# Kernel tuning notes

Measured on AMD Instinct MI355X. Metric: run time of the kernel, lower is better.

## Reference

```python
import jax, jax.numpy as jnp
import numpy as np

MAX_SEQ = 768  # hardcoded in original compute_freqs_cis
THETA = 10000.0


def _freqs_cis(C, T):
    # freqs over FULL embed dim C (matches original, not per-head)
    freqs = 1.0 / THETA ** (jnp.arange(0, C, 2, dtype=jnp.float32)[: C // 2] / C)
    t = jnp.arange(MAX_SEQ, dtype=jnp.float32)
    ang = jnp.outer(t, freqs)  # [MAX_SEQ, C/2]
    return jnp.cos(ang)[:T], jnp.sin(ang)[:T]  # each [T, C/2]


def _apply_rope(u):
    # u: [B, T, C]; rotate adjacent channel pairs across full C
    B, T, C = u.shape
    fr, fi = _freqs_cis(C, T)           # [T, C/2]
    u2 = u.astype(jnp.float32).reshape(B, T, C // 2, 2)
    ur, ui = u2[..., 0], u2[..., 1]     # [B, T, C/2]
    out_r = ur * fr - ui * fi
    out_i = ur * fi + ui * fr
    return jnp.stack([out_r, out_i], axis=-1).reshape(B, T, C).astype(u.dtype)


def setup_inputs() -> dict:
    key = jax.random.key(0)
    k1, k2, k3 = jax.random.split(key, 3)
    B, T, C = 16, 768, 1024
    x = jax.random.normal(k1, (B, T, C), dtype=jnp.float32)
    Wqkv = jax.random.normal(k2, (3 * C, C), dtype=jnp.float32) * 0.02
    bqkv = jnp.zeros((3 * C,), dtype=jnp.float32)
    Wo = jax.random.normal(k3, (C, C), dtype=jnp.float32) * 0.02
    bo = jnp.zeros((C,), dtype=jnp.float32)
    return {"x": x, "Wqkv": Wqkv, "bqkv": bqkv, "Wo": Wo, "bo": bo}


def reference(x, Wqkv, bqkv, Wo, bo):
    B, T, C = x.shape
    H = 16
    D = C // H
    qkv = x @ Wqkv.T + bqkv                      # [B, T, 3C]
    q, k, v = jnp.split(qkv, 3, axis=-1)
    q = _apply_rope(q)
    k = _apply_rope(k)
    # [B, H, T, D]
    q = q.reshape(B, T, H, D).transpose(0, 2, 1, 3)
    k = k.reshape(B, T, H, D).transpose(0, 2, 1, 3)
    v = v.reshape(B, T, H, D).transpose(0, 2, 1, 3)
    scale = 1.0 / jnp.sqrt(jnp.asarray(D, dtype=q.dtype))
    scores = jnp.einsum("bhqd,bhkd->bhqk", q, k) * scale
    causal = jnp.tril(jnp.ones((T, T), dtype=bool))
    scores = jnp.where(causal, scores, jnp.finfo(scores.dtype).min)
    attn = jax.nn.softmax(scores, axis=-1)
    y = jnp.einsum("bhqk,bhkd->bhqd", attn, v)   # [B, H, T, D]
    y = y.transpose(0, 2, 1, 3).reshape(B, T, C)
    return y @ Wo.T + bo
```

## Files before the change

### kernel.cpp

```cpp
#include <hip/hip_runtime.h>
#include <hip/hip_bf16.h>

typedef __attribute__((ext_vector_type(8))) short bf16x8;
typedef __attribute__((ext_vector_type(4))) float f32x4;
typedef unsigned short u16;
typedef unsigned int u32;

#define DEV __device__ __forceinline__

DEV float bf2f(u16 v) { u32 u = ((u32)v) << 16; return __builtin_bit_cast(float, u); }
DEV u16 f2bf(float f) {
    u32 u = __builtin_bit_cast(u32, f);
    u32 r = (u + 0x7FFFu + ((u >> 16) & 1u)) >> 16;
    return (u16)r;
}

DEV void gll16(const u16* g, u16* l) {
    __builtin_amdgcn_global_load_lds((const __attribute__((address_space(1))) void*)g,
                                     (__attribute__((address_space(3))) void*)l, 16, 0, 0);
}

#define WAIT_VM0()   asm volatile("s_waitcnt vmcnt(0)" ::: "memory")
#define WAIT_LGKM0() asm volatile("s_waitcnt lgkmcnt(0)" ::: "memory")
#define BAR()        __builtin_amdgcn_s_barrier()
#define BARF()       asm volatile("s_barrier" ::: "memory")

__global__ void detect_kernel(const u32* __restrict__ x, int* __restrict__ flag) {
    __shared__ int cnt;
    if (threadIdx.x == 0) cnt = 0;
    __syncthreads();
    int c = 0;
    for (int i = threadIdx.x; i < 4096; i += 256) {
        u32 w = x[i];
        u32 e = (w >> 7) & 0xFF;
        c += (e >= 110 && e <= 132) ? 1 : 0;
    }
    atomicAdd(&cnt, c);
    __syncthreads();
    if (threadIdx.x == 0) *flag = (cnt * 2 > 4096) ? 1 : 0;
}

__global__ void cvt_bf16_kernel(const void* __restrict__ in, u16* __restrict__ out,
                                int n8, const int* __restrict__ flag) {
    const int fl = *flag;
    int i = blockIdx.x * 256 + threadIdx.x;
    const int stride = gridDim.x * 256;
    if (fl) {
        const bf16x8* ip = (const bf16x8*)in;
        bf16x8* op = (bf16x8*)out;
        for (; i < n8; i += stride) op[i] = ip[i];
    } else {
        const float4* ip = (const float4*)in;
        bf16x8* op = (bf16x8*)out;
        for (; i < n8; i += stride) {
            float4 a = ip[2 * i], b = ip[2 * i + 1];
            bf16x8 o;
            o[0] = (short)f2bf(a.x); o[1] = (short)f2bf(a.y);
            o[2] = (short)f2bf(a.z); o[3] = (short)f2bf(a.w);
            o[4] = (short)f2bf(b.x); o[5] = (short)f2bf(b.y);
            o[6] = (short)f2bf(b.z); o[7] = (short)f2bf(b.w);
            op[i] = o;
        }
    }
}

__global__ void cvt_f32_kernel(const void* __restrict__ in, float* __restrict__ out,
                               int n, const int* __restrict__ flag) {
    const int fl = *flag;
    int i = blockIdx.x * 256 + threadIdx.x;
    if (i < n) out[i] = fl ? bf2f(((const u16*)in)[i]) : ((const float*)in)[i];
}

__global__ void rope_table_kernel(float2* __restrict__ tab) {
    int idx = blockIdx.x * 256 + threadIdx.x;
    int t = idx >> 9, j = idx & 511;
    float freq = expf(-(float)(2 * j) * (9.210340371976184f / 1024.0f));
    float ang = (float)t * freq;
    tab[idx] = make_float2(cosf(ang), sinf(ang));
}

__global__ __launch_bounds__(256)
void gemm128_kernel(const u16* __restrict__ A, const u16* __restrict__ W,
                    const float* __restrict__ bias, void* __restrict__ C,
                    int N, const int* __restrict__ flag, int out_mode,
                    const float2* __restrict__ tab, int rope) {
    constexpr int K = 1024, NT = 16;
    __shared__ u16 lds[2][16384];
    const int tid = threadIdx.x;
    const int l = tid & 63, w = tid >> 6;
    const int wm = w >> 1, wn = w & 1;
    const int lo = l & 15, hi = l >> 4;

    const int M0 = blockIdx.x * 128, N0 = blockIdx.y * 128;

    const int rS = tid >> 3;
    const int qS = (tid & 7) ^ (rS & 7);
    const u16* Ag = A + (size_t)(M0 + rS) * K + qS * 8;
    const u16* Wg = W + (size_t)(N0 + rS) * K + qS * 8;
    const int lb = w * 512;

    f32x4 acc[4][4] = {};

#define STAGE(kt, slot)                                                        \
    {                                                                          \
        u16* sA = &lds[slot][0];                                               \
        u16* sB = &lds[slot][8192];                                            \
        const u16* ga = Ag + (kt) * 64;                                        \
        const u16* gb = Wg + (kt) * 64;                                        \
        gll16(ga,                   sA + lb);                                  \
        gll16(ga + (size_t)32 * K,  sA + 2048 + lb);                           \
        gll16(ga + (size_t)64 * K,  sA + 4096 + lb);                           \
        gll16(ga + (size_t)96 * K,  sA + 6144 + lb);                           \
        gll16(gb,                   sB + lb);                                  \
        gll16(gb + (size_t)32 * K,  sB + 2048 + lb);                           \
        gll16(gb + (size_t)64 * K,  sB + 4096 + lb);                           \
        gll16(gb + (size_t)96 * K,  sB + 6144 + lb);                           \
    }

    STAGE(0, 0);
    WAIT_VM0();
    BARF();

#pragma unroll 1
    for (int j = 0; j < NT; ++j) {
        const int cur = j & 1;
        if (j + 1 < NT) STAGE(j + 1, cur ^ 1);

        const u16* sA = &lds[cur][0];
        const u16* sB = &lds[cur][8192];
        bf16x8 a[4][2], b[4][2];
#pragma unroll
        for (int m = 0; m < 4; ++m)
#pragma unroll
            for (int ks = 0; ks < 2; ++ks)
                a[m][ks] = *(const bf16x8*)&sA[(wm * 64 + m * 16 + lo) * 64 +
                                               (((ks * 4 + hi) ^ (lo & 7)) * 8)];
#pragma unroll
        for (int n = 0; n < 4; ++n)
#pragma unroll
            for (int ks = 0; ks < 2; ++ks)
                b[n][ks] = *(const bf16x8*)&sB[(wn * 64 + n * 16 + lo) * 64 +
                                               (((ks * 4 + hi) ^ (lo & 7)) * 8)];
        __builtin_amdgcn_s_setprio(1);
#pragma unroll
        for (int m = 0; m < 4; ++m)
#pragma unroll
            for (int n = 0; n < 4; ++n)
#pragma unroll
                for (int ks = 0; ks < 2; ++ks)
                    acc[m][n] = __builtin_amdgcn_mfma_f32_16x16x32_bf16(a[m][ks], b[n][ks], acc[m][n], 0, 0, 0);
        __builtin_amdgcn_s_setprio(0);

        if (j + 1 < NT) WAIT_VM0();
        BARF();
    }
#undef STAGE

    const int f32out = out_mode ? (*flag == 0) : 0;
    const int do_rope = rope && (N0 < 2048);
    const int row0 = M0 + wm * 64 + hi * 4;
    const int col0 = N0 + wn * 64 + lo;
    const int t0 = (M0 % 768) + wm * 64 + hi * 4;
#pragma unroll
    for (int n = 0; n < 4; ++n) {
        const int col = col0 + n * 16;
        float bi = bias[col];
        const int jf = (col & 1023) >> 1;
        const int odd = col & 1;
#pragma unroll
        for (int m = 0; m < 4; ++m)
#pragma unroll
            for (int j = 0; j < 4; ++j) {
                float v = acc[m][n][j] + bi;
                if (do_rope) {
                    float partner = __shfl_xor(v, 1);
                    float2 cs = tab[(t0 + m * 16 + j) * 512 + jf];
                    v = odd ? (v * cs.x + partner * cs.y) : (v * cs.x - partner * cs.y);
                }
                size_t idx = (size_t)(row0 + m * 16 + j) * N + col;
                if (f32out) ((float*)C)[idx] = v;
                else        ((u16*)C)[idx] = f2bf(v);
            }
    }
}

__global__ __launch_bounds__(256)
void attn_kernel(const u16* __restrict__ qkv, u16* __restrict__ y) {
    constexpr int T = 768, CH = 1024, QKVC = 3072;
    constexpr float NEG = -30000.0f;
    __shared__ u16 Ks[2][64 * 64];
    __shared__ u16 Vt[64 * 72];
    __shared__ u16 Ps[64 * 72];

    const int tid = threadIdx.x, l = tid & 63, w = tid >> 6;
    const int qt = blockIdx.x, h = blockIdx.y, b = blockIdx.z;
    const int lo = l & 15, hi = l >> 4;
    const int kk = hi * 8;
    const int swzk = (lo & 7) * 8;

    const int qrow = qt * 64 + w * 16 + lo;
    const u16* qptr = qkv + (size_t)(b * T + qrow) * QKVC + h * 64 + kk;
    bf16x8 aq0r = *(const bf16x8*)qptr;
    bf16x8 aq1r = *(const bf16x8*)(qptr + 32);
    bf16x8 aq0, aq1;
#pragma unroll
    for (int e = 0; e < 8; ++e) {
        aq0[e] = (short)f2bf(bf2f((u16)aq0r[e]) * 0.125f);
        aq1[e] = (short)f2bf(bf2f((u16)aq1r[e]) * 0.125f);
    }

    f32x4 o[4] = {};
    float mrun[4] = {NEG, NEG, NEG, NEG};
    float lrun[4] = {0.f, 0.f, 0.f, 0.f};

    const int ksr = w * 16 + (l >> 3);
    const int ksc = ((l & 7) ^ ((l >> 3) & 7)) * 8;
    const u16* kbase = qkv + (size_t)(b * T + ksr) * QKVC + CH + h * 64 + ksc;

    const int vd0 = (tid & 7) * 8;
    const int vswz = (tid & 7) * 8;
    const int vr0 = tid >> 3, vr1 = 32 + (tid >> 3);
    const u16* vbase = qkv + (size_t)(b * T) * QKVC + 2 * CH + h * 64 + vd0;

    gll16(kbase, &Ks[0][w * 1024]);
    gll16(kbase + (size_t)8 * QKVC, &Ks[0][w * 1024 + 512]);
    bf16x8 cv0 = *(const bf16x8*)(vbase + (size_t)vr0 * QKVC);
    bf16x8 cv1 = *(const bf16x8*)(vbase + (size_t)vr1 * QKVC);
    WAIT_VM0();
#pragma unroll
    for (int e = 0; e < 8; ++e) {
        Vt[(vd0 + e) * 72 + (vr0 ^ vswz)] = (u16)cv0[e];
        Vt[(vd0 + e) * 72 + (vr1 ^ vswz)] = (u16)cv1[e];
    }

    for (int kt = 0; kt <= qt; ++kt) {
        const int cur = kt & 1, nxt = cur ^ 1;
        bf16x8 nv0, nv1;
        if (kt < qt) {
            const size_t koff = (size_t)((kt + 1) * 64) * QKVC;
            gll16(kbase + koff, &Ks[nxt][w * 1024]);
            gll16(kbase + koff + (size_t)8 * QKVC, &Ks[nxt][w * 1024 + 512]);
            const u16* vb2 = vbase + (size_t)((kt + 1) * 64) * QKVC;
            nv0 = *(const bf16x8*)(vb2 + (size_t)vr0 * QKVC);
            nv1 = *(const bf16x8*)(vb2 + (size_t)vr1 * QKVC);
        }
        WAIT_LGKM0();
        BAR();

        __builtin_amdgcn_s_setprio(1);
        f32x4 s[4];
#pragma unroll
        for (int n = 0; n < 4; ++n) {
            bf16x8 kb0 = *(const bf16x8*)&Ks[cur][(n * 16 + lo) * 64 + (kk ^ swzk)];
            bf16x8 kb1 = *(const bf16x8*)&Ks[cur][(n * 16 + lo) * 64 + ((32 + kk) ^ swzk)];
            f32x4 z = {0.f, 0.f, 0.f, 0.f};
            z = __builtin_amdgcn_mfma_f32_16x16x32_bf16(aq0, kb0, z, 0, 0, 0);
            z = __builtin_amdgcn_mfma_f32_16x16x32_bf16(aq1, kb1, z, 0, 0, 0);
            s[n] = z;
        }
        __builtin_amdgcn_s_setprio(0);

        if (kt == qt) {
#pragma unroll
            for (int n = 0; n < 4; ++n) {
                int kcol = n * 16 + lo;
#pragma unroll
                for (int j = 0; j < 4; ++j)
                    if (kcol > w * 16 + hi * 4 + j) s[n][j] = NEG;
            }
        }
        float mnew[4], corr[4];
#pragma unroll
        for (int j = 0; j < 4; ++j) {
            float mx = fmaxf(fmaxf(s[0][j], s[1][j]), fmaxf(s[2][j], s[3][j]));
            mx = fmaxf(mx, __shfl_xor(mx, 1));
            mx = fmaxf(mx, __shfl_xor(mx, 2));
            mx = fmaxf(mx, __shfl_xor(mx, 4));
            mx = fmaxf(mx, __shfl_xor(mx, 8));
            mnew[j] = fmaxf(mrun[j], mx);
            corr[j] = __expf(mrun[j] - mnew[j]);
            mrun[j] = mnew[j];
        }
        float p[4][4];
#pragma unroll
        for (int n = 0; n < 4; ++n)
#pragma unroll
            for (int j = 0; j < 4; ++j)
                p[n][j] = __expf(s[n][j] - mnew[j]);
#pragma unroll
        for (int j = 0; j < 4; ++j) {
            float r = p[0][j] + p[1][j] + p[2][j] + p[3][j];
            r += __shfl_xor(r, 1);
            r += __shfl_xor(r, 2);
            r += __shfl_xor(r, 4);
            r += __shfl_xor(r, 8);
            lrun[j] = lrun[j] * corr[j] + r;
        }
#pragma unroll
        for (int n = 0; n < 4; ++n)
#pragma unroll
            for (int j = 0; j < 4; ++j)
                o[n][j] *= corr[j];
#pragma unroll
        for (int n = 0; n < 4; ++n)
#pragma unroll
            for (int j = 0; j < 4; ++j)
                Ps[(w * 16 + hi * 4 + j) * 72 + n * 16 + lo] = f2bf(p[n][j]);

        __builtin_amdgcn_s_setprio(1);
#pragma unroll
        for (int c = 0; c < 2; ++c) {
            bf16x8 pa = *(const bf16x8*)&Ps[(w * 16 + lo) * 72 + c * 32 + kk];
#pragma unroll
            for (int n = 0; n < 4; ++n) {
                const int v = (n * 2 + (lo >> 3)) & 7;
                bf16x8 vb = *(const bf16x8*)&Vt[(n * 16 + lo) * 72 + ((c * 32 + kk) ^ (v * 8))];
                o[n] = __builtin_amdgcn_mfma_f32_16x16x32_bf16(pa, vb, o[n], 0, 0, 0);
            }
        }
        __builtin_amdgcn_s_setprio(0);

        if (kt < qt) {
            WAIT_VM0();
            BAR();
#pragma unroll
            for (int e = 0; e < 8; ++e) {
                Vt[(vd0 + e) * 72 + (vr0 ^ vswz)] = (u16)nv0[e];
                Vt[(vd0 + e) * 72 + (vr1 ^ vswz)] = (u16)nv1[e];
            }
        }
    }

    float inv[4];
#pragma unroll
    for (int j = 0; j < 4; ++j) inv[j] = (lrun[j] > 0.f) ? 1.0f / lrun[j] : 0.f;
#pragma unroll
    for (int n = 0; n < 4; ++n)
#pragma unroll
        for (int j = 0; j < 4; ++j) {
            int t = qt * 64 + w * 16 + hi * 4 + j;
            y[(size_t)(b * T + t) * CH + h * 64 + n * 16 + lo] = f2bf(o[n][j] * inv[j]);
        }
}

extern "C" void kernel_launch(void* const* d_in, const int* in_sizes, int n_in,
                              void* d_out, int out_size, void* d_ws, size_t ws_size,
                              hipStream_t stream) {
    char* ws = (char*)d_ws;
    int*   flag  = (int*)ws;
    u16*   xb    = (u16*)(ws + 256);
    u16*   Wqb   = (u16*)(ws + 256 + 25165824);
    u16*   Wob   = (u16*)(ws + 256 + 31457280);
    float* bqf   = (float*)(ws + 256 + 33554432);
    float* bof   = (float*)(ws + 256 + 33566720);
    u16*   qkv   = (u16*)(ws + 256 + 33570816);
    u16*   y     = (u16*)(ws + 256 + 109068288);
    float2* tab  = (float2*)(ws + 256 + 134234112);

    detect_kernel<<<1, 256, 0, stream>>>((const u32*)d_in[0], flag);
    cvt_bf16_kernel<<<2048, 256, 0, stream>>>(d_in[0], xb,  12582912 / 8, flag);
    cvt_bf16_kernel<<<1536, 256, 0, stream>>>(d_in[1], Wqb, 3145728 / 8, flag);
    cvt_bf16_kernel<<<512,  256, 0, stream>>>(d_in[3], Wob, 1048576 / 8, flag);
    cvt_f32_kernel<<<12, 256, 0, stream>>>(d_in[2], bqf, 3072, flag);
    cvt_f32_kernel<<<4,  256, 0, stream>>>(d_in[4], bof, 1024, flag);
    rope_table_kernel<<<768 * 512 / 256, 256, 0, stream>>>(tab);

    gemm128_kernel<<<dim3(96, 24), 256, 0, stream>>>(xb, Wqb, bqf, qkv, 3072, flag, 0, tab, 1);
    attn_kernel<<<dim3(12, 16, 16), 256, 0, stream>>>(qkv, y);
    gemm128_kernel<<<dim3(96, 8), 256, 0, stream>>>(y, Wob, bof, d_out, 1024, flag, 1, tab, 0);
}
```

Measured before the change: 316.3 us.

## Use 256x128 tile GEMM with triple-buffered LDS for QKV projection

Adds a 512-thread GEMM kernel with a 256x128 output tile and a three-slot LDS ring that prefetches two K-tiles ahead, using a partial vmcnt wait instead of a full drain. It replaces the 128x128 kernel for the QKV projection. The aim is more reuse of each W tile per block and better overlap of global loads with MFMA work. In exchange it uses about 144KB of LDS per block, which may cap occupancy at one block per CU, and launches half as many blocks.

```diff
diff --git a/kernel.cpp b/kernel.cpp
--- a/kernel.cpp
+++ b/kernel.cpp
@@ -21,6 +21,7 @@
 }
 
 #define WAIT_VM0()   asm volatile("s_waitcnt vmcnt(0)" ::: "memory")
+#define WAIT_VM6()   asm volatile("s_waitcnt vmcnt(6)" ::: "memory")
 #define WAIT_LGKM0() asm volatile("s_waitcnt lgkmcnt(0)" ::: "memory")
 #define BAR()        __builtin_amdgcn_s_barrier()
 #define BARF()       asm volatile("s_barrier" ::: "memory")
@@ -79,6 +80,110 @@
     tab[idx] = make_float2(cosf(ang), sinf(ang));
 }
 
+__global__ __launch_bounds__(512)
+void gemm256_kernel(const u16* __restrict__ A, const u16* __restrict__ W,
+                    const float* __restrict__ bias, void* __restrict__ C,
+                    int N, const int* __restrict__ flag, int out_mode,
+                    const float2* __restrict__ tab, int rope) {
+    constexpr int K = 1024, NT = 16;
+    __shared__ u16 lds[3][24576];
+    const int tid = threadIdx.x;
+    const int l = tid & 63, w = tid >> 6;
+    const int wm = w >> 1, wn = w & 1;
+    const int lo = l & 15, hi = l >> 4;
+
+    const int M0 = blockIdx.x * 256, N0 = blockIdx.y * 128;
+
+    const int rS = tid >> 3;
+    const int qS = (tid & 7) ^ (rS & 7);
+    const u16* Ag = A + (size_t)(M0 + rS) * K + qS * 8;
+    const u16* Wg = W + (size_t)(N0 + rS) * K + qS * 8;
+    const int lb = w * 512;
+
+    f32x4 acc[4][4] = {};
+
+#define STAGE(kt, slot)                                                        \
+    {                                                                          \
+        u16* sA = &lds[slot][0];                                               \
+        u16* sB = &lds[slot][16384];                                           \
+        const u16* ga = Ag + (kt) * 64;                                        \
+        const u16* gb = Wg + (kt) * 64;                                        \
+        gll16(ga,                       sA + lb);                              \
+        gll16(ga + (size_t)64 * K,      sA + 4096 + lb);                       \
+        gll16(ga + (size_t)128 * K,     sA + 8192 + lb);                       \
+        gll16(ga + (size_t)192 * K,     sA + 12288 + lb);                      \
+        gll16(gb,                       sB + lb);                              \
+        gll16(gb + (size_t)64 * K,      sB + 4096 + lb);                       \
+    }
+
+    STAGE(0, 0);
+    STAGE(1, 1);
+    WAIT_VM6();
+
+#pragma unroll 1
+    for (int j = 0; j < NT; ++j) {
+        BAR();
+        if (j + 2 < NT) {
+            STAGE(j + 2, (j + 2) % 3);
+            WAIT_VM6();
+        } else {
+            WAIT_VM0();
+        }
+        const u16* sA = &lds[j % 3][0];
+        const u16* sB = &lds[j % 3][16384];
+        bf16x8 a[4][2], b[4][2];
+#pragma unroll
+        for (int m = 0; m < 4; ++m)
+#pragma unroll
+            for (int ks = 0; ks < 2; ++ks)
+                a[m][ks] = *(const bf16x8*)&sA[(wm * 64 + m * 16 + lo) * 64 +
+                                               (((ks * 4 + hi) ^ (lo & 7)) * 8)];
+#pragma unroll
+        for (int n = 0; n < 4; ++n)
+#pragma unroll
+            for (int ks = 0; ks < 2; ++ks)
+                b[n][ks] = *(const bf16x8*)&sB[(wn * 64 + n * 16 + lo) * 64 +
+                                               (((ks * 4 + hi) ^ (lo & 7)) * 8)];
+        __builtin_amdgcn_s_setprio(1);
+#pragma unroll
+        for (int m = 0; m < 4; ++m)
+#pragma unroll
+            for (int n = 0; n < 4; ++n)
+#pragma unroll
+                for (int ks = 0; ks < 2; ++ks)
+                    acc[m][n] = __builtin_amdgcn_mfma_f32_16x16x32_bf16(a[m][ks], b[n][ks], acc[m][n], 0, 0, 0);
+        __builtin_amdgcn_s_setprio(0);
+    }
+#undef STAGE
+
+    const int f32out = out_mode ? (*flag == 0) : 0;
+    const int do_rope = rope && (N0 < 2048);
+    const int row0 = M0 + wm * 64 + hi * 4;
+    const int col0 = N0 + wn * 64 + lo;
+    const int t0 = (M0 % 768) + wm * 64 + hi * 4;
+#pragma unroll
+    for (int n = 0; n < 4; ++n) {
+        const int col = col0 + n * 16;
+        float bi = bias[col];
+        const int jf = (col & 1023) >> 1;
+        const int odd = col & 1;
+#pragma unroll
+        for (int m = 0; m < 4; ++m)
+#pragma unroll
+            for (int j = 0; j < 4; ++j) {
+                float v = acc[m][n][j] + bi;
+                if (do_rope) {
+                    float partner = __shfl_xor(v, 1);
+                    float2 cs = tab[(t0 + m * 16 + j) * 512 + jf];
+                    v = odd ? (v * cs.x + partner * cs.y) : (v * cs.x - partner * cs.y);
+                }
+                size_t idx = (size_t)(row0 + m * 16 + j) * N + col;
+                if (f32out) ((float*)C)[idx] = v;
+                else        ((u16*)C)[idx] = f2bf(v);
+            }
+    }
+}
+
 __global__ __launch_bounds__(256)
 void gemm128_kernel(const u16* __restrict__ A, const u16* __restrict__ W,
                     const float* __restrict__ bias, void* __restrict__ C,
@@ -365,7 +470,7 @@
     cvt_f32_kernel<<<4,  256, 0, stream>>>(d_in[4], bof, 1024, flag);
     rope_table_kernel<<<768 * 512 / 256, 256, 0, stream>>>(tab);
 
-    gemm128_kernel<<<dim3(96, 24), 256, 0, stream>>>(xb, Wqb, bqf, qkv, 3072, flag, 0, tab, 1);
+    gemm256_kernel<<<dim3(48, 24), 512, 0, stream>>>(xb, Wqb, bqf, qkv, 3072, flag, 0, tab, 1);
     attn_kernel<<<dim3(12, 16, 16), 256, 0, stream>>>(qkv, y);
     gemm128_kernel<<<dim3(96, 8), 256, 0, stream>>>(y, Wob, bof, d_out, 1024, flag, 1, tab, 0);
 }
```

New measurement: 325.2 us. 1.03x slower.

## Replace 128x128 GEMM with 256x256 tile, 8-wave ping-pong pipelined kernel

Applied to the files above, without the earlier changes.

The QKV and output projection GEMMs move from a 128x128 tile with 4 waves to a 256x256 tile with 8 waves, and each wave now computes 128x64. The K-loop is split into four MFMA phases separated by barriers, with the A and B loads for the next stage issued between phases so loads overlap compute. The aim is more operand reuse per LDS byte and better latency hiding. In exchange the kernel needs 128KB of LDS per block and more accumulator registers, and it launches fewer blocks (576 and 192), so wave quantization across CUs is a risk, especially for the output GEMM.

```diff
diff --git a/kernel.cpp b/kernel.cpp
--- a/kernel.cpp
+++ b/kernel.cpp
@@ -79,19 +79,19 @@
     tab[idx] = make_float2(cosf(ang), sinf(ang));
 }
 
-__global__ __launch_bounds__(256)
-void gemm128_kernel(const u16* __restrict__ A, const u16* __restrict__ W,
-                    const float* __restrict__ bias, void* __restrict__ C,
-                    int N, const int* __restrict__ flag, int out_mode,
-                    const float2* __restrict__ tab, int rope) {
+__global__ __launch_bounds__(512, 2)
+void gemm256p_kernel(const u16* __restrict__ A, const u16* __restrict__ W,
+                     const float* __restrict__ bias, void* __restrict__ C,
+                     int N, const int* __restrict__ flag, int out_mode,
+                     const float2* __restrict__ tab, int rope) {
     constexpr int K = 1024, NT = 16;
-    __shared__ u16 lds[2][16384];
+    __shared__ u16 lds[2][32768];
     const int tid = threadIdx.x;
     const int l = tid & 63, w = tid >> 6;
-    const int wm = w >> 1, wn = w & 1;
+    const int wm = w >> 2, wn = w & 3;
     const int lo = l & 15, hi = l >> 4;
 
-    const int M0 = blockIdx.x * 128, N0 = blockIdx.y * 128;
+    const int M0 = blockIdx.x * 256, N0 = blockIdx.y * 256;
 
     const int rS = tid >> 3;
     const int qS = (tid & 7) ^ (rS & 7);
@@ -99,88 +99,126 @@
     const u16* Wg = W + (size_t)(N0 + rS) * K + qS * 8;
     const int lb = w * 512;
 
-    f32x4 acc[4][4] = {};
-
-#define STAGE(kt, slot)                                                        \
+    f32x4 acc[8][4] = {};
+
+#define STG_A(kt, slot, half)                                                  \
     {                                                                          \
-        u16* sA = &lds[slot][0];                                               \
-        u16* sB = &lds[slot][8192];                                            \
-        const u16* ga = Ag + (kt) * 64;                                        \
-        const u16* gb = Wg + (kt) * 64;                                        \
-        gll16(ga,                   sA + lb);                                  \
-        gll16(ga + (size_t)32 * K,  sA + 2048 + lb);                           \
-        gll16(ga + (size_t)64 * K,  sA + 4096 + lb);                           \
-        gll16(ga + (size_t)96 * K,  sA + 6144 + lb);                           \
-        gll16(gb,                   sB + lb);                                  \
-        gll16(gb + (size_t)32 * K,  sB + 2048 + lb);                           \
-        gll16(gb + (size_t)64 * K,  sB + 4096 + lb);                           \
-        gll16(gb + (size_t)96 * K,  sB + 6144 + lb);                           \
-    }
-
-    STAGE(0, 0);
+        u16* sA_ = &lds[slot][(half) * 8192];                                  \
+        const u16* ga_ = Ag + (kt) * 64 + (size_t)(128 * (half)) * K;          \
+        gll16(ga_,                  sA_ + lb);                                 \
+        gll16(ga_ + (size_t)64 * K, sA_ + 4096 + lb);                          \
+    }
+#define STG_B(kt, slot, half)                                                  \
+    {                                                                          \
+        u16* sB_ = &lds[slot][16384 + (half) * 8192];                          \
+        const u16* gb_ = Wg + (kt) * 64 + (size_t)(128 * (half)) * K;          \
+        gll16(gb_,                  sB_ + lb);                                 \
+        gll16(gb_ + (size_t)64 * K, sB_ + 4096 + lb);                          \
+    }
+
+    STG_A(0, 0, 0); STG_A(0, 0, 1);
+    STG_B(0, 0, 0); STG_B(0, 0, 1);
     WAIT_VM0();
     BARF();
 
+    const int csw = lo & 7;
+
 #pragma unroll 1
-    for (int j = 0; j < NT; ++j) {
-        const int cur = j & 1;
-        if (j + 1 < NT) STAGE(j + 1, cur ^ 1);
-
+    for (int t = 0; t < NT; ++t) {
+        const int cur = t & 1, nxt = cur ^ 1;
         const u16* sA = &lds[cur][0];
-        const u16* sB = &lds[cur][8192];
-        bf16x8 a[4][2], b[4][2];
-#pragma unroll
-        for (int m = 0; m < 4; ++m)
-#pragma unroll
-            for (int ks = 0; ks < 2; ++ks)
-                a[m][ks] = *(const bf16x8*)&sA[(wm * 64 + m * 16 + lo) * 64 +
-                                               (((ks * 4 + hi) ^ (lo & 7)) * 8)];
+        const u16* sB = &lds[cur][16384];
+        bf16x8 afr[4], bfr[4];
+
 #pragma unroll
         for (int n = 0; n < 4; ++n)
-#pragma unroll
-            for (int ks = 0; ks < 2; ++ks)
-                b[n][ks] = *(const bf16x8*)&sB[(wn * 64 + n * 16 + lo) * 64 +
-                                               (((ks * 4 + hi) ^ (lo & 7)) * 8)];
+            bfr[n] = *(const bf16x8*)&sB[(wn * 64 + n * 16 + lo) * 64 + ((hi ^ csw) * 8)];
+#pragma unroll
+        for (int m = 0; m < 4; ++m)
+            afr[m] = *(const bf16x8*)&sA[(wm * 128 + m * 16 + lo) * 64 + ((hi ^ csw) * 8)];
+        if (t + 1 < NT) { STG_A(t + 1, nxt, 0); STG_A(t + 1, nxt, 1); }
+        BARF();
         __builtin_amdgcn_s_setprio(1);
 #pragma unroll
         for (int m = 0; m < 4; ++m)
 #pragma unroll
             for (int n = 0; n < 4; ++n)
-#pragma unroll
-                for (int ks = 0; ks < 2; ++ks)
-                    acc[m][n] = __builtin_amdgcn_mfma_f32_16x16x32_bf16(a[m][ks], b[n][ks], acc[m][n], 0, 0, 0);
-        __builtin_amdgcn_s_setprio(0);
-
-        if (j + 1 < NT) WAIT_VM0();
-        BARF();
-    }
-#undef STAGE
+                acc[m][n] = __builtin_amdgcn_mfma_f32_16x16x32_bf16(afr[m], bfr[n], acc[m][n], 0, 0, 0);
+        __builtin_amdgcn_s_setprio(0);
+        BARF();
+
+#pragma unroll
+        for (int m = 0; m < 4; ++m)
+            afr[m] = *(const bf16x8*)&sA[(wm * 128 + 64 + m * 16 + lo) * 64 + ((hi ^ csw) * 8)];
+        if (t + 1 < NT) { STG_B(t + 1, nxt, 0); STG_B(t + 1, nxt, 1); }
+        BARF();
+        __builtin_amdgcn_s_setprio(1);
+#pragma unroll
+        for (int m = 0; m < 4; ++m)
+#pragma unroll
+            for (int n = 0; n < 4; ++n)
+                acc[4 + m][n] = __builtin_amdgcn_mfma_f32_16x16x32_bf16(afr[m], bfr[n], acc[4 + m][n], 0, 0, 0);
+        __builtin_amdgcn_s_setprio(0);
+        BARF();
+
+#pragma unroll
+        for (int n = 0; n < 4; ++n)
+            bfr[n] = *(const bf16x8*)&sB[(wn * 64 + n * 16 + lo) * 64 + (((4 + hi) ^ csw) * 8)];
+#pragma unroll
+        for (int m = 0; m < 4; ++m)
+            afr[m] = *(const bf16x8*)&sA[(wm * 128 + m * 16 + lo) * 64 + (((4 + hi) ^ csw) * 8)];
+        BARF();
+        __builtin_amdgcn_s_setprio(1);
+#pragma unroll
+        for (int m = 0; m < 4; ++m)
+#pragma unroll
+            for (int n = 0; n < 4; ++n)
+                acc[m][n] = __builtin_amdgcn_mfma_f32_16x16x32_bf16(afr[m], bfr[n], acc[m][n], 0, 0, 0);
+        __builtin_amdgcn_s_setprio(0);
+        BARF();
+
+#pragma unroll
+        for (int m = 0; m < 4; ++m)
+            afr[m] = *(const bf16x8*)&sA[(wm * 128 + 64 + m * 16 + lo) * 64 + (((4 + hi) ^ csw) * 8)];
+        WAIT_VM0();
+        BARF();
+        __builtin_amdgcn_s_setprio(1);
+#pragma unroll
+        for (int m = 0; m < 4; ++m)
+#pragma unroll
+            for (int n = 0; n < 4; ++n)
+                acc[4 + m][n] = __builtin_amdgcn_mfma_f32_16x16x32_bf16(afr[m], bfr[n], acc[4 + m][n], 0, 0, 0);
+        __builtin_amdgcn_s_setprio(0);
+        BARF();
+    }
+#undef STG_A
+#undef STG_B
 
     const int f32out = out_mode ? (*flag == 0) : 0;
     const int do_rope = rope && (N0 < 2048);
-    const int row0 = M0 + wm * 64 + hi * 4;
-    const int col0 = N0 + wn * 64 + lo;
-    const int t0 = (M0 % 768) + wm * 64 + hi * 4;
-#pragma unroll
-    for (int n = 0; n < 4; ++n) {
-        const int col = col0 + n * 16;
-        float bi = bias[col];
-        const int jf = (col & 1023) >> 1;
-        const int odd = col & 1;
-#pragma unroll
-        for (int m = 0; m < 4; ++m)
+#pragma unroll
+    for (int mi = 0; mi < 8; ++mi) {
+        const int rbase = M0 + wm * 128 + (mi >> 2) * 64 + (mi & 3) * 16 + hi * 4;
+        const int tbase = (M0 % 768) + wm * 128 + (mi >> 2) * 64 + (mi & 3) * 16 + hi * 4;
+#pragma unroll
+        for (int n = 0; n < 4; ++n) {
+            const int col = N0 + wn * 64 + lo + n * 16;
+            float bi = bias[col];
+            const int jf = (col & 1023) >> 1;
+            const int odd = col & 1;
 #pragma unroll
             for (int j = 0; j < 4; ++j) {
-                float v = acc[m][n][j] + bi;
+                float v = acc[mi][n][j] + bi;
                 if (do_rope) {
                     float partner = __shfl_xor(v, 1);
-                    float2 cs = tab[(t0 + m * 16 + j) * 512 + jf];
+                    float2 cs = tab[(tbase + j) * 512 + jf];
                     v = odd ? (v * cs.x + partner * cs.y) : (v * cs.x - partner * cs.y);
                 }
-                size_t idx = (size_t)(row0 + m * 16 + j) * N + col;
+                size_t idx = (size_t)(rbase + j) * N + col;
                 if (f32out) ((float*)C)[idx] = v;
                 else        ((u16*)C)[idx] = f2bf(v);
             }
+        }
     }
 }
 
@@ -365,7 +403,7 @@
     cvt_f32_kernel<<<4,  256, 0, stream>>>(d_in[4], bof, 1024, flag);
     rope_table_kernel<<<768 * 512 / 256, 256, 0, stream>>>(tab);
 
-    gemm128_kernel<<<dim3(96, 24), 256, 0, stream>>>(xb, Wqb, bqf, qkv, 3072, flag, 0, tab, 1);
+    gemm256p_kernel<<<dim3(48, 12), 512, 0, stream>>>(xb, Wqb, bqf, qkv, 3072, flag, 0, tab, 1);
     attn_kernel<<<dim3(12, 16, 16), 256, 0, stream>>>(qkv, y);
-    gemm128_kernel<<<dim3(96, 8), 256, 0, stream>>>(y, Wob, bof, d_out, 1024, flag, 1, tab, 0);
-}
+    gemm256p_kernel<<<dim3(48, 4), 512, 0, stream>>>(y, Wob, bof, d_out, 1024, flag, 1, tab, 0);
+}
```

Result: faster. 308.4 us (-2.5%).
